# Optimization experiments

Hardware: AMD Instinct MI355X
Metric: run time of the kernel (lower is better)

## Reference

```python
import jax, jax.numpy as jnp
import numpy as np
from math import gcd

N_SIG = 2097152   # signal length
L_FILT = 129      # FIR taps


def setup_inputs() -> dict:
    key = jax.random.key(0)
    k1, k2 = jax.random.split(key)
    x = jax.random.normal(k1, (N_SIG,), dtype=jnp.float32)
    h = jax.random.normal(k2, (L_FILT,), dtype=jnp.float32)
    return {"x": x, "h": h, "up": 3, "down": 2}


def _get_start_index(length):
    if length <= 2:
        return 0
    return (length - 1) // 2


def reference(x, h, up, down):
    # Reduce rates by gcd, as in the torch module.
    g = gcd(up, down)
    up, down = up // g, down // g
    if up == 1 and down == 1:
        return x
    N = x.shape[0]
    L = h.shape[0]
    # zero-stuff: x_up[::up] = up * x  (gain `up` matches resample_poly)
    x_up = jnp.zeros(up * N, dtype=x.dtype).at[::up].set(up * x)
    # full FIR convolution, then phase-offset strided downsample
    full = jnp.convolve(x_up, h.astype(x.dtype), mode="full")  # [up*N + L - 1]
    start = _get_start_index(L)
    n_out = -(-(N * up) // down)  # ceil(N*up/down)
    return full[start::down][:n_out]
```

## Files before the change

### kernel.cpp

```cpp
#include <hip/hip_runtime.h>


#define N_SIG   2097152
#define L_FILT  129
#define NTAPS   43
#define G       2
#define BLK     256
#define GROUPS_PER_BLK (BLK * G)
#define TILE_Q  1088

template <int U, int RP>
__device__ __forceinline__ void do_chunk(const float* __restrict__ xs,
                                         const float* __restrict__ h,
                                         int i0, int tid, float (&acc)[3 * G]) {
    const int D = 45 - (i0 + U - 1);
    constexpr int NW = (RP + U + 2 * G - 1 + 3) >> 2;
    const float* base = xs + 4 * tid + (D - RP);
    float4 vec[NW];
#pragma unroll
    for (int m = 0; m < NW; ++m)
        vec[m] = *(const float4*)(base + 4 * m);
    const float* vf = (const float*)vec;
#pragma unroll
    for (int u = 0; u < U; ++u) {
        const float h0 = h[3 * (i0 + u) + 0];
        const float h1 = h[3 * (i0 + u) + 1];
        const float h2 = h[3 * (i0 + u) + 2];
#pragma unroll
        for (int g = 0; g < G; ++g) {
            const float xa = vf[RP + (U - 1 - u) + 2 * g];
            const float xb = vf[RP + (U - 1 - u) + 2 * g + 1];
            acc[3 * g + 0] += xa * h1;
            acc[3 * g + 1] += xb * h0;
            acc[3 * g + 2] += xb * h2;
        }
    }
}

__global__ __launch_bounds__(BLK, 8) void poly_kernel(
    const float* __restrict__ x, const float* __restrict__ h,
    float* __restrict__ out, int n_out)
{
    __shared__ float xs[TILE_Q];

    const int tid = threadIdx.x;
    const int b   = blockIdx.x;

    const int tb = 2 * GROUPS_PER_BLK * b - 24;

    for (int q4 = tid; q4 < TILE_Q / 4; q4 += BLK) {
        const int gx = tb + 4 * q4;
        float4 v;
        if (gx >= 0 && gx + 3 < N_SIG) {
            v = *(const float4*)(x + gx);
        } else {
            v.x = (gx     >= 0 && gx     < N_SIG) ? x[gx]     : 0.0f;
            v.y = (gx + 1 >= 0 && gx + 1 < N_SIG) ? x[gx + 1] : 0.0f;
            v.z = (gx + 2 >= 0 && gx + 2 < N_SIG) ? x[gx + 2] : 0.0f;
            v.w = (gx + 3 >= 0 && gx + 3 < N_SIG) ? x[gx + 3] : 0.0f;
        }
        *(float4*)(xs + 4 * q4) = v;
    }
    __syncthreads();

    float acc[3 * G];
#pragma unroll
    for (int k = 0; k < 3 * G; ++k) acc[k] = 0.0f;

#pragma unroll 1
    for (int i0 = 0; i0 < 32; i0 += 16)
        do_chunk<16, 2>(xs, h, i0, tid, acc);
    __builtin_amdgcn_sched_barrier(0);
    do_chunk<11, 3>(xs, h, 32, tid, acc);

    const int ob = 3 * GROUPS_PER_BLK * b + 3 * G * tid;
#pragma unroll
    for (int k = 0; k < 3; ++k) {
        if (ob + 2 * k + 1 < n_out) {
            *(float2*)(out + ob + 2 * k) =
                make_float2(3.0f * acc[2 * k + 0], 3.0f * acc[2 * k + 1]);
        }
    }
}

extern "C" void kernel_launch(void* const* d_in, const int* in_sizes, int n_in,
                              void* d_out, int out_size, void* d_ws, size_t ws_size,
                              hipStream_t stream) {
    const float* x = (const float*)d_in[0];
    const float* h = (const float*)d_in[1];
    float* out = (float*)d_out;
    const int blocks = (out_size + 3 * GROUPS_PER_BLK - 1) / (3 * GROUPS_PER_BLK);
    poly_kernel<<<blocks, BLK, 0, stream>>>(x, h, out, out_size);
}
```

Measured before the change: 73.53 us.

## Drop LDS staging and read input windows directly from global memory

Removes the shared-memory tile and the block-wide barrier. Each thread now loads its overlapping float4 windows straight from global memory, relying on the L1/L2 caches to serve the reuse between neighbouring threads. Edge blocks use a templated guarded path for the boundary checks. This saves the LDS store/load round trip and the sync, but it multiplies global load instructions, since each input element is fetched by several threads, and it drops the sched_barrier.

Result: no change. 73.97 us (+0.6%).

```diff
diff --git a/kernel.cpp b/kernel.cpp
--- a/kernel.cpp
+++ b/kernel.cpp
@@ -7,19 +7,31 @@
 #define G       2
 #define BLK     256
 #define GROUPS_PER_BLK (BLK * G)
-#define TILE_Q  1088
 
-template <int U, int RP>
-__device__ __forceinline__ void do_chunk(const float* __restrict__ xs,
+__device__ __forceinline__ float ldg_guard(const float* __restrict__ x, int gx) {
+    return (gx >= 0 && gx < N_SIG) ? x[gx] : 0.0f;
+}
+
+template <int U, int RP, bool EDGE>
+__device__ __forceinline__ void do_chunk(const float* __restrict__ x,
                                          const float* __restrict__ h,
-                                         int i0, int tid, float (&acc)[3 * G]) {
+                                         int i0, int gbase0, float (&acc)[3 * G]) {
     const int D = 45 - (i0 + U - 1);
     constexpr int NW = (RP + U + 2 * G - 1 + 3) >> 2;
-    const float* base = xs + 4 * tid + (D - RP);
+    const int gb = gbase0 + (D - RP);
     float4 vec[NW];
 #pragma unroll
-    for (int m = 0; m < NW; ++m)
-        vec[m] = *(const float4*)(base + 4 * m);
+    for (int m = 0; m < NW; ++m) {
+        const int gx = gb + 4 * m;
+        if (!EDGE) {
+            vec[m] = *(const float4*)(x + gx);
+        } else {
+            vec[m].x = ldg_guard(x, gx);
+            vec[m].y = ldg_guard(x, gx + 1);
+            vec[m].z = ldg_guard(x, gx + 2);
+            vec[m].w = ldg_guard(x, gx + 3);
+        }
+    }
     const float* vf = (const float*)vec;
 #pragma unroll
     for (int u = 0; u < U; ++u) {
@@ -41,37 +53,26 @@
     const float* __restrict__ x, const float* __restrict__ h,
     float* __restrict__ out, int n_out)
 {
-    __shared__ float xs[TILE_Q];
-
     const int tid = threadIdx.x;
     const int b   = blockIdx.x;
 
-    const int tb = 2 * GROUPS_PER_BLK * b - 24;
-
-    for (int q4 = tid; q4 < TILE_Q / 4; q4 += BLK) {
-        const int gx = tb + 4 * q4;
-        float4 v;
-        if (gx >= 0 && gx + 3 < N_SIG) {
-            v = *(const float4*)(x + gx);
-        } else {
-            v.x = (gx     >= 0 && gx     < N_SIG) ? x[gx]     : 0.0f;
-            v.y = (gx + 1 >= 0 && gx + 1 < N_SIG) ? x[gx + 1] : 0.0f;
-            v.z = (gx + 2 >= 0 && gx + 2 < N_SIG) ? x[gx + 2] : 0.0f;
-            v.w = (gx + 3 >= 0 && gx + 3 < N_SIG) ? x[gx + 3] : 0.0f;
-        }
-        *(float4*)(xs + 4 * q4) = v;
-    }
-    __syncthreads();
+    const int gbase0 = 2 * GROUPS_PER_BLK * b - 24 + 4 * tid;
 
     float acc[3 * G];
 #pragma unroll
     for (int k = 0; k < 3 * G; ++k) acc[k] = 0.0f;
 
+    if (b != 0 && b != (int)gridDim.x - 1) {
 #pragma unroll 1
-    for (int i0 = 0; i0 < 32; i0 += 16)
-        do_chunk<16, 2>(xs, h, i0, tid, acc);
-    __builtin_amdgcn_sched_barrier(0);
-    do_chunk<11, 3>(xs, h, 32, tid, acc);
+        for (int i0 = 0; i0 < 32; i0 += 16)
+            do_chunk<16, 2, false>(x, h, i0, gbase0, acc);
+        do_chunk<11, 3, false>(x, h, 32, gbase0, acc);
+    } else {
+#pragma unroll 1
+        for (int i0 = 0; i0 < 32; i0 += 16)
+            do_chunk<16, 2, true>(x, h, i0, gbase0, acc);
+        do_chunk<11, 3, true>(x, h, 32, gbase0, acc);
+    }
 
     const int ob = 3 * GROUPS_PER_BLK * b + 3 * G * tid;
 #pragma unroll
```
